# Kernel tuning notes

Hardware: AMD Instinct MI355X
Metric: run time of the kernel (lower is better)

The kernel has to match this reference:

```python
import jax, jax.numpy as jnp
import numpy as np

N_NODES = 100000
N_EDGES = 3200000
IN_DIM = 256
HID = 128
OUT = 2
BN_EPS = 1e-5


def setup_inputs() -> dict:
    key = jax.random.key(0)
    ks = jax.random.split(key, 4)
    x = jax.random.normal(ks[0], (N_NODES, IN_DIM), dtype=jnp.float32)
    edge_index = jax.random.randint(ks[1], (2, N_EDGES), 0, N_NODES, dtype=jnp.int64)
    # Glorot-ish scaled weights
    W1 = jax.random.normal(ks[2], (IN_DIM, HID), dtype=jnp.float32) * (1.0 / np.sqrt(IN_DIM))
    W2 = jax.random.normal(ks[3], (HID, OUT), dtype=jnp.float32) * (1.0 / np.sqrt(HID))
    return {
        "x": x,
        "edge_index": edge_index,
        "feature_importance": jnp.ones((IN_DIM,), jnp.float32),
        "W1": W1,
        "b1": jnp.zeros((HID,), jnp.float32),
        "W2": W2,
        "b2": jnp.zeros((OUT,), jnp.float32),
        "gamma": jnp.ones((HID,), jnp.float32),
        "beta": jnp.zeros((HID,), jnp.float32),
    }


def _gcn_conv(x, row, col, norm, W, b, n_nodes):
    # PyG GCNConv: linear transform then D^-1/2 (A+I) D^-1/2 aggregation
    h = x @ W  # [N, d_out]
    msg = h[row] * norm[:, None]  # gather + scale, [E+N, d_out]
    out = jax.ops.segment_sum(msg, col, num_segments=n_nodes)  # scatter-add
    return out + b


def _norm_and_loops(edge_index, n_nodes, dtype):
    loop = jnp.arange(n_nodes, dtype=edge_index.dtype)
    row = jnp.concatenate([edge_index[0], loop])
    col = jnp.concatenate([edge_index[1], loop])
    deg = jax.ops.segment_sum(jnp.ones_like(col, dtype=dtype), col, num_segments=n_nodes)
    dinv = jnp.where(deg > 0, jax.lax.rsqrt(deg), 0.0)
    norm = dinv[row] * dinv[col]
    return row, col, norm


def reference(x, edge_index, feature_importance, W1, b1, W2, b2, gamma, beta):
    n_nodes = x.shape[0]
    row, col, norm = _norm_and_loops(edge_index, n_nodes, x.dtype)
    # sigmoid feature-importance weighting
    xw = x * jax.nn.sigmoid(feature_importance)
    h = _gcn_conv(xw, row, col, norm, W1, b1, n_nodes)
    # BatchNorm1d with batch statistics (training-mode math; dropout omitted = eval)
    mu = jnp.mean(h, axis=0)
    var = jnp.mean((h - mu) ** 2, axis=0)
    h = (h - mu) * jax.lax.rsqrt(var + BN_EPS) * gamma + beta
    h = jax.nn.relu(h)
    out = _gcn_conv(h, row, col, norm, W2, b2, n_nodes)
    return out
```

## Files before the change

kernel.cpp:

```cpp
#include <hip/hip_runtime.h>
#include <hip/hip_bf16.h>

#define N_NODES 100000
#define N_EDGES 3200000
#define IN_DIM 256
#define HID 128
#define BN_EPS 1e-5f
#define SCAN_B 1024
#define NB1 ((N_NODES + SCAN_B - 1) / SCAN_B)


__global__ void k_deg(const int* __restrict__ col, unsigned* __restrict__ cnt) {
    int i = blockIdx.x * blockDim.x + threadIdx.x;
    if (i < N_EDGES) atomicAdd(&cnt[col[i]], 1u);
}

__global__ void k_dinv(const unsigned* __restrict__ cnt, float* __restrict__ dinv) {
    int i = blockIdx.x * blockDim.x + threadIdx.x;
    if (i < N_NODES) dinv[i] = rsqrtf((float)(cnt[i] + 1u));
}

__global__ void k_sig(const float* __restrict__ fi, float* __restrict__ sig) {
    int i = threadIdx.x;
    if (i < IN_DIM) sig[i] = 1.0f / (1.0f + expf(-fi[i]));
}


__global__ __launch_bounds__(SCAN_B) void k_scan_part(const unsigned* __restrict__ cnt,
                                                      unsigned* __restrict__ rowptr,
                                                      unsigned* __restrict__ blocksum) {
    __shared__ unsigned s[SCAN_B];
    int t = threadIdx.x;
    int i = blockIdx.x * SCAN_B + t;
    unsigned v = (i < N_NODES) ? cnt[i] : 0u;
    s[t] = v;
    __syncthreads();
#pragma unroll
    for (int off = 1; off < SCAN_B; off <<= 1) {
        unsigned u = (t >= off) ? s[t - off] : 0u;
        __syncthreads();
        s[t] += u;
        __syncthreads();
    }
    if (i < N_NODES) rowptr[i] = s[t] - v;
    if (t == SCAN_B - 1) blocksum[blockIdx.x] = s[t];
}

__global__ __launch_bounds__(128) void k_scan_mid(const unsigned* __restrict__ blocksum,
                                                  unsigned* __restrict__ blockoff) {
    __shared__ unsigned s[128];
    int t = threadIdx.x;
    unsigned v = (t < NB1) ? blocksum[t] : 0u;
    s[t] = v;
    __syncthreads();
#pragma unroll
    for (int off = 1; off < 128; off <<= 1) {
        unsigned u = (t >= off) ? s[t - off] : 0u;
        __syncthreads();
        s[t] += u;
        __syncthreads();
    }
    if (t < NB1) blockoff[t] = s[t] - v;
}

__global__ void k_scan_add(unsigned* __restrict__ rowptr, const unsigned* __restrict__ blockoff) {
    int i = blockIdx.x * blockDim.x + threadIdx.x;
    if (i < N_NODES) rowptr[i] += blockoff[i >> 10];
    if (i == 0) rowptr[N_NODES] = N_EDGES;
}


__global__ void k_bucket(const int* __restrict__ row, const int* __restrict__ col,
                         const unsigned* __restrict__ rowptr, unsigned* __restrict__ fill,
                         int* __restrict__ esrc) {
    int e = blockIdx.x * blockDim.x + threadIdx.x;
    if (e < N_EDGES) {
        int c = col[e];
        unsigned p = rowptr[c] + atomicAdd(&fill[c], 1u);
        esrc[p] = row[e];
    }
}


__global__ __launch_bounds__(256) void k_gemm1(const float* __restrict__ x,
                                               const float* __restrict__ W1,
                                               const float* __restrict__ sig,
                                               const float* __restrict__ dinv,
                                               float* __restrict__ hs) {
    __shared__ float xT[16][64];
    __shared__ float Wl[16][128];
    const int mbase = blockIdx.x * 64;
    const int t = threadIdx.x;
    const int tm = t >> 5;
    const int tn = t & 31;
    float acc[8][4] = {{0.f}};

    for (int k0 = 0; k0 < IN_DIM; k0 += 16) {
        {
            int r = t >> 2;
            int kk = (t & 3) * 4;
            int row = mbase + r;
            float4 v = make_float4(0.f, 0.f, 0.f, 0.f);
            if (row < N_NODES) v = *(const float4*)&x[row * IN_DIM + k0 + kk];
            xT[kk + 0][r] = v.x; xT[kk + 1][r] = v.y;
            xT[kk + 2][r] = v.z; xT[kk + 3][r] = v.w;
        }
        {
#pragma unroll
            for (int i = 0; i < 2; ++i) {
                int idx = t + i * 256;
                int k = idx >> 5;
                int n4 = (idx & 31) * 4;
                float4 w = *(const float4*)&W1[(k0 + k) * HID + n4];
                float s = sig[k0 + k];
                Wl[k][n4 + 0] = w.x * s; Wl[k][n4 + 1] = w.y * s;
                Wl[k][n4 + 2] = w.z * s; Wl[k][n4 + 3] = w.w * s;
            }
        }
        __syncthreads();
#pragma unroll
        for (int k = 0; k < 16; ++k) {
            float xv[8], wv[4];
            *(float4*)&xv[0] = *(const float4*)&xT[k][tm * 8];
            *(float4*)&xv[4] = *(const float4*)&xT[k][tm * 8 + 4];
            *(float4*)&wv[0] = *(const float4*)&Wl[k][tn * 4];
#pragma unroll
            for (int i = 0; i < 8; ++i)
#pragma unroll
                for (int j = 0; j < 4; ++j)
                    acc[i][j] += xv[i] * wv[j];
        }
        __syncthreads();
    }
#pragma unroll
    for (int i = 0; i < 8; ++i) {
        int row = mbase + tm * 8 + i;
        if (row < N_NODES) {
            float d = dinv[row];
            float4 v = make_float4(acc[i][0] * d, acc[i][1] * d, acc[i][2] * d, acc[i][3] * d);
            *(float4*)&hs[row * HID + tn * 4] = v;
        }
    }
}


__global__ __launch_bounds__(256) void k_agg1csr(const int* __restrict__ esrc,
                                                 const unsigned* __restrict__ rowptr,
                                                 const float* __restrict__ hs,
                                                 const float* __restrict__ dinv,
                                                 const float* __restrict__ b1,
                                                 float* __restrict__ S1,
                                                 float* __restrict__ stats) {
    const int t = threadIdx.x;
    const int lane = t & 63;
    const int gw = (blockIdx.x * blockDim.x + t) >> 6;
    const int nw = (gridDim.x * blockDim.x) >> 6;
    const int ch = lane * 2;
    const float2 bb = *(const float2*)&b1[ch];
    float s0 = 0.f, s1 = 0.f, q0 = 0.f, q1 = 0.f;

    for (int c = gw; c < N_NODES; c += nw) {
        unsigned beg = rowptr[c], end = rowptr[c + 1];
        float2 acc = *(const float2*)&hs[(size_t)c * HID + ch];
        for (unsigned base = beg; base < end; base += 64) {
            int n = (int)min(64u, end - base);
            int my = (lane < n) ? esrc[base + lane] : 0;
#pragma unroll 4
            for (int i = 0; i < n; ++i) {
                int r = __shfl(my, i);
                float2 v = *(const float2*)&hs[(size_t)r * HID + ch];
                acc.x += v.x; acc.y += v.y;
            }
        }
        float d = dinv[c];
        float v0 = d * acc.x + bb.x;
        float v1 = d * acc.y + bb.y;
        *(float2*)&S1[(size_t)c * HID + ch] = make_float2(v0, v1);
        s0 += v0; s1 += v1; q0 += v0 * v0; q1 += v1 * v1;
    }

    __shared__ float red[256];
#define RED_ATOMIC(val, idx)                                              \
    red[t] = (val); __syncthreads();                                      \
    if (t < 64) {                                                         \
        float r_ = red[t] + red[t + 64] + red[t + 128] + red[t + 192];    \
        atomicAdd(&stats[idx], r_);                                       \
    } __syncthreads();
    RED_ATOMIC(s0, ch)
    RED_ATOMIC(s1, ch + 1)
    RED_ATOMIC(q0, 128 + ch)
    RED_ATOMIC(q1, 129 + ch)
#undef RED_ATOMIC
}


__global__ void k_bnfin(const float* __restrict__ stats,
                        const float* __restrict__ gamma,
                        const float* __restrict__ beta,
                        float* __restrict__ bnp) {
    int j = threadIdx.x;
    if (j < HID) {
        float mu = stats[j] * (1.0f / N_NODES);
        float var = stats[128 + j] * (1.0f / N_NODES) - mu * mu;
        float rstd = rsqrtf(var + BN_EPS);
        float sc = rstd * gamma[j];
        bnp[j] = sc;
        bnp[128 + j] = beta[j] - mu * sc;
    }
}


__global__ __launch_bounds__(256) void k_gemm2(const float* __restrict__ S1,
                                               const float* __restrict__ bnp,
                                               const float* __restrict__ W2,
                                               const float* __restrict__ dinv,
                                               float* __restrict__ gs) {
    int wid = (blockIdx.x * blockDim.x + threadIdx.x) >> 6;
    int lane = threadIdx.x & 63;
    int nw = (gridDim.x * blockDim.x) >> 6;
    int k0 = lane * 2;
    float2 sc = *(const float2*)&bnp[k0];
    float2 sh = *(const float2*)&bnp[128 + k0];
    float4 w = *(const float4*)&W2[k0 * 2];
    for (int n = wid; n < N_NODES; n += nw) {
        float2 h = *(const float2*)&S1[(size_t)n * HID + k0];
        float v0 = fmaxf(h.x * sc.x + sh.x, 0.f);
        float v1 = fmaxf(h.y * sc.y + sh.y, 0.f);
        float a0 = v0 * w.x + v1 * w.z;
        float a1 = v0 * w.y + v1 * w.w;
#pragma unroll
        for (int off = 32; off; off >>= 1) {
            a0 += __shfl_down(a0, off);
            a1 += __shfl_down(a1, off);
        }
        if (lane == 0) {
            float d = dinv[n];
            *(float2*)&gs[n * 2] = make_float2(a0 * d, a1 * d);
        }
    }
}


__global__ void k_agg2csr(const int* __restrict__ esrc,
                          const unsigned* __restrict__ rowptr,
                          const float* __restrict__ gs,
                          const float* __restrict__ dinv,
                          const float* __restrict__ b2,
                          float* __restrict__ out) {
    int c = blockIdx.x * blockDim.x + threadIdx.x;
    if (c >= N_NODES) return;
    float2 acc = *(const float2*)&gs[c * 2];
    unsigned beg = rowptr[c], end = rowptr[c + 1];
    for (unsigned i = beg; i < end; ++i) {
        int r = esrc[i];
        float2 v = *(const float2*)&gs[r * 2];
        acc.x += v.x; acc.y += v.y;
    }
    float d = dinv[c];
    *(float2*)&out[c * 2] = make_float2(d * acc.x + b2[0], d * acc.y + b2[1]);
}


extern "C" void kernel_launch(void* const* d_in, const int* in_sizes, int n_in,
                              void* d_out, int out_size, void* d_ws, size_t ws_size,
                              hipStream_t stream) {
    const float* x     = (const float*)d_in[0];
    const int*   edge  = (const int*)d_in[1];
    const float* fi    = (const float*)d_in[2];
    const float* W1    = (const float*)d_in[3];
    const float* b1    = (const float*)d_in[4];
    const float* W2    = (const float*)d_in[5];
    const float* b2    = (const float*)d_in[6];
    const float* gamma = (const float*)d_in[7];
    const float* beta  = (const float*)d_in[8];
    float* out = (float*)d_out;

    const int* erow = edge;
    const int* ecol = edge + N_EDGES;

    char* ws = (char*)d_ws;
    size_t off = 0;
    auto alloc = [&](size_t bytes) { size_t r = off; off = (off + bytes + 255) & ~(size_t)255; return r; };
    float*    hs    = (float*)(ws + alloc(sizeof(float) * (size_t)N_NODES * HID));
    float*    S1    = (float*)(ws + alloc(sizeof(float) * (size_t)N_NODES * HID));
    int*      esrc  = (int*)(ws + alloc(sizeof(int) * (size_t)N_EDGES));
    float*    gs    = (float*)(ws + alloc(sizeof(float) * N_NODES * 2));
    unsigned* cnt   = (unsigned*)(ws + alloc(sizeof(unsigned) * N_NODES));
    unsigned* fill  = (unsigned*)(ws + alloc(sizeof(unsigned) * N_NODES));
    unsigned* rowptr= (unsigned*)(ws + alloc(sizeof(unsigned) * (N_NODES + 1)));
    unsigned* bsum  = (unsigned*)(ws + alloc(sizeof(unsigned) * NB1));
    unsigned* boff  = (unsigned*)(ws + alloc(sizeof(unsigned) * NB1));
    float*    dinv  = (float*)(ws + alloc(sizeof(float) * N_NODES));
    float*    sig   = (float*)(ws + alloc(sizeof(float) * IN_DIM));
    float*    stats = (float*)(ws + alloc(sizeof(float) * 2 * HID));
    float*    bnp   = (float*)(ws + alloc(sizeof(float) * 2 * HID));
    (void)ws_size; (void)in_sizes; (void)n_in; (void)out_size;

    hipMemsetAsync(cnt, 0, sizeof(unsigned) * N_NODES, stream);
    hipMemsetAsync(fill, 0, sizeof(unsigned) * N_NODES, stream);
    hipMemsetAsync(stats, 0, sizeof(float) * 2 * HID, stream);

    k_deg<<<(N_EDGES + 255) / 256, 256, 0, stream>>>(ecol, cnt);
    k_dinv<<<(N_NODES + 255) / 256, 256, 0, stream>>>(cnt, dinv);
    k_sig<<<1, 256, 0, stream>>>(fi, sig);

    k_scan_part<<<NB1, SCAN_B, 0, stream>>>(cnt, rowptr, bsum);
    k_scan_mid<<<1, 128, 0, stream>>>(bsum, boff);
    k_scan_add<<<(N_NODES + 255) / 256, 256, 0, stream>>>(rowptr, boff);
    k_bucket<<<(N_EDGES + 255) / 256, 256, 0, stream>>>(erow, ecol, rowptr, fill, esrc);

    k_gemm1<<<(N_NODES + 63) / 64, 256, 0, stream>>>(x, W1, sig, dinv, hs);
    k_agg1csr<<<2048, 256, 0, stream>>>(esrc, rowptr, hs, dinv, b1, S1, stats);
    k_bnfin<<<1, 128, 0, stream>>>(stats, gamma, beta, bnp);
    k_gemm2<<<2048, 256, 0, stream>>>(S1, bnp, W2, dinv, gs);
    k_agg2csr<<<(N_NODES + 255) / 256, 256, 0, stream>>>(esrc, rowptr, gs, dinv, b2, out);
}
```

Baseline: 895.6 us.

## Use bf16 MFMA for first GEMM and store hidden features as bf16

Replaces the fp32 shared-memory SIMT GEMM with bf16 MFMA 16x16x32 instructions. The sigmoid-scaled W1 is pre-transposed and converted to bf16 in a small prep kernel, and x is converted to bf16 on the fly. The hidden features hs are now written as packed bf16, which halves the bytes gathered per edge in the first aggregation, the dominant memory-bound gather over 3.2M edges. In exchange, precision drops to bf16 in both the GEMM inputs and the stored intermediate features.

Result: faster. 822.4 us (-8.2%).

```diff
diff --git a/kernel.cpp b/kernel.cpp
--- a/kernel.cpp
+++ b/kernel.cpp
@@ -9,6 +9,17 @@
 #define SCAN_B 1024
 #define NB1 ((N_NODES + SCAN_B - 1) / SCAN_B)
 
+typedef __attribute__((ext_vector_type(8))) short bf16x8;
+typedef __attribute__((ext_vector_type(4))) float f32x4;
+
+__device__ __forceinline__ ushort f2bf(float f) {
+    unsigned u = __float_as_uint(f);
+    u += 0x7FFFu + ((u >> 16) & 1u);
+    return (ushort)(u >> 16);
+}
+__device__ __forceinline__ float bflo(unsigned v) { return __uint_as_float(v << 16); }
+__device__ __forceinline__ float bfhi(unsigned v) { return __uint_as_float(v & 0xFFFF0000u); }
+
 
 __global__ void k_deg(const int* __restrict__ col, unsigned* __restrict__ cnt) {
     int i = blockIdx.x * blockDim.x + threadIdx.x;
@@ -23,6 +34,15 @@
 __global__ void k_sig(const float* __restrict__ fi, float* __restrict__ sig) {
     int i = threadIdx.x;
     if (i < IN_DIM) sig[i] = 1.0f / (1.0f + expf(-fi[i]));
+}
+
+__global__ void k_prepw(const float* __restrict__ W1, const float* __restrict__ sig,
+                        ushort* __restrict__ W1t) {
+    int idx = blockIdx.x * blockDim.x + threadIdx.x;
+    if (idx < HID * IN_DIM) {
+        int n = idx >> 8, k = idx & 255;
+        W1t[idx] = f2bf(W1[k * HID + n] * sig[k]);
+    }
 }
 
 
@@ -83,70 +103,51 @@
 
 
 __global__ __launch_bounds__(256) void k_gemm1(const float* __restrict__ x,
-                                               const float* __restrict__ W1,
-                                               const float* __restrict__ sig,
+                                               const ushort* __restrict__ W1t,
                                                const float* __restrict__ dinv,
-                                               float* __restrict__ hs) {
-    __shared__ float xT[16][64];
-    __shared__ float Wl[16][128];
-    const int mbase = blockIdx.x * 64;
+                                               unsigned* __restrict__ hsu) {
     const int t = threadIdx.x;
-    const int tm = t >> 5;
-    const int tn = t & 31;
-    float acc[8][4] = {{0.f}};
-
-    for (int k0 = 0; k0 < IN_DIM; k0 += 16) {
-        {
-            int r = t >> 2;
-            int kk = (t & 3) * 4;
-            int row = mbase + r;
-            float4 v = make_float4(0.f, 0.f, 0.f, 0.f);
-            if (row < N_NODES) v = *(const float4*)&x[row * IN_DIM + k0 + kk];
-            xT[kk + 0][r] = v.x; xT[kk + 1][r] = v.y;
-            xT[kk + 2][r] = v.z; xT[kk + 3][r] = v.w;
+    const int w = (blockIdx.x << 2) + (t >> 6);
+    const int m0 = w << 4;
+    if (m0 >= N_NODES) return;
+    const int lane = t & 63;
+    const int mrow = lane & 15;
+    const int quad = lane >> 4;
+
+    const float* xrow = x + (size_t)(m0 + mrow) * IN_DIM + quad * 8;
+    const ushort* wrow = W1t + mrow * IN_DIM + quad * 8;
+
+    f32x4 acc[8] = {};
+#pragma unroll
+    for (int ks = 0; ks < 8; ++ks) {
+        float4 xa = *(const float4*)(xrow + ks * 32);
+        float4 xb = *(const float4*)(xrow + ks * 32 + 4);
+        bf16x8 bfrag;
+        bfrag[0] = (short)f2bf(xa.x); bfrag[1] = (short)f2bf(xa.y);
+        bfrag[2] = (short)f2bf(xa.z); bfrag[3] = (short)f2bf(xa.w);
+        bfrag[4] = (short)f2bf(xb.x); bfrag[5] = (short)f2bf(xb.y);
+        bfrag[6] = (short)f2bf(xb.z); bfrag[7] = (short)f2bf(xb.w);
+        const ushort* wk = wrow + ks * 32;
+#pragma unroll
+        for (int nb = 0; nb < 8; ++nb) {
+            bf16x8 afrag = *(const bf16x8*)(wk + nb * 16 * IN_DIM);
+            acc[nb] = __builtin_amdgcn_mfma_f32_16x16x32_bf16(afrag, bfrag, acc[nb], 0, 0, 0);
         }
-        {
-#pragma unroll
-            for (int i = 0; i < 2; ++i) {
-                int idx = t + i * 256;
-                int k = idx >> 5;
-                int n4 = (idx & 31) * 4;
-                float4 w = *(const float4*)&W1[(k0 + k) * HID + n4];
-                float s = sig[k0 + k];
-                Wl[k][n4 + 0] = w.x * s; Wl[k][n4 + 1] = w.y * s;
-                Wl[k][n4 + 2] = w.z * s; Wl[k][n4 + 3] = w.w * s;
-            }
-        }
-        __syncthreads();
-#pragma unroll
-        for (int k = 0; k < 16; ++k) {
-            float xv[8], wv[4];
-            *(float4*)&xv[0] = *(const float4*)&xT[k][tm * 8];
-            *(float4*)&xv[4] = *(const float4*)&xT[k][tm * 8 + 4];
-            *(float4*)&wv[0] = *(const float4*)&Wl[k][tn * 4];
-#pragma unroll
-            for (int i = 0; i < 8; ++i)
-#pragma unroll
-                for (int j = 0; j < 4; ++j)
-                    acc[i][j] += xv[i] * wv[j];
-        }
-        __syncthreads();
-    }
-#pragma unroll
-    for (int i = 0; i < 8; ++i) {
-        int row = mbase + tm * 8 + i;
-        if (row < N_NODES) {
-            float d = dinv[row];
-            float4 v = make_float4(acc[i][0] * d, acc[i][1] * d, acc[i][2] * d, acc[i][3] * d);
-            *(float4*)&hs[row * HID + tn * 4] = v;
-        }
+    }
+    const float d = dinv[m0 + mrow];
+    unsigned* orow = hsu + (size_t)(m0 + mrow) * 64;
+#pragma unroll
+    for (int nb = 0; nb < 8; ++nb) {
+        unsigned p0 = (unsigned)f2bf(acc[nb][0] * d) | ((unsigned)f2bf(acc[nb][1] * d) << 16);
+        unsigned p1 = (unsigned)f2bf(acc[nb][2] * d) | ((unsigned)f2bf(acc[nb][3] * d) << 16);
+        *(uint2*)(orow + nb * 8 + quad * 2) = make_uint2(p0, p1);
     }
 }
 
 
 __global__ __launch_bounds__(256) void k_agg1csr(const int* __restrict__ esrc,
                                                  const unsigned* __restrict__ rowptr,
-                                                 const float* __restrict__ hs,
+                                                 const unsigned* __restrict__ hsu,
                                                  const float* __restrict__ dinv,
                                                  const float* __restrict__ b1,
                                                  float* __restrict__ S1,
@@ -161,20 +162,21 @@
 
     for (int c = gw; c < N_NODES; c += nw) {
         unsigned beg = rowptr[c], end = rowptr[c + 1];
-        float2 acc = *(const float2*)&hs[(size_t)c * HID + ch];
+        unsigned self = hsu[(size_t)c * 64 + lane];
+        float a0 = bflo(self), a1 = bfhi(self);
         for (unsigned base = beg; base < end; base += 64) {
             int n = (int)min(64u, end - base);
             int my = (lane < n) ? esrc[base + lane] : 0;
 #pragma unroll 4
             for (int i = 0; i < n; ++i) {
                 int r = __shfl(my, i);
-                float2 v = *(const float2*)&hs[(size_t)r * HID + ch];
-                acc.x += v.x; acc.y += v.y;
+                unsigned v = hsu[(size_t)r * 64 + lane];
+                a0 += bflo(v); a1 += bfhi(v);
             }
         }
         float d = dinv[c];
-        float v0 = d * acc.x + bb.x;
-        float v1 = d * acc.y + bb.y;
+        float v0 = d * a0 + bb.x;
+        float v1 = d * a1 + bb.y;
         *(float2*)&S1[(size_t)c * HID + ch] = make_float2(v0, v1);
         s0 += v0; s1 += v1; q0 += v0 * v0; q1 += v1 * v1;
     }
@@ -281,7 +283,7 @@
     char* ws = (char*)d_ws;
     size_t off = 0;
     auto alloc = [&](size_t bytes) { size_t r = off; off = (off + bytes + 255) & ~(size_t)255; return r; };
-    float*    hs    = (float*)(ws + alloc(sizeof(float) * (size_t)N_NODES * HID));
+    unsigned* hsu   = (unsigned*)(ws + alloc(sizeof(unsigned) * (size_t)N_NODES * 64));
     float*    S1    = (float*)(ws + alloc(sizeof(float) * (size_t)N_NODES * HID));
     int*      esrc  = (int*)(ws + alloc(sizeof(int) * (size_t)N_EDGES));
     float*    gs    = (float*)(ws + alloc(sizeof(float) * N_NODES * 2));
@@ -292,6 +294,7 @@
     unsigned* boff  = (unsigned*)(ws + alloc(sizeof(unsigned) * NB1));
     float*    dinv  = (float*)(ws + alloc(sizeof(float) * N_NODES));
     float*    sig   = (float*)(ws + alloc(sizeof(float) * IN_DIM));
+    ushort*   W1t   = (ushort*)(ws + alloc(sizeof(ushort) * HID * IN_DIM));
     float*    stats = (float*)(ws + alloc(sizeof(float) * 2 * HID));
     float*    bnp   = (float*)(ws + alloc(sizeof(float) * 2 * HID));
     (void)ws_size; (void)in_sizes; (void)n_in; (void)out_size;
@@ -303,14 +306,15 @@
     k_deg<<<(N_EDGES + 255) / 256, 256, 0, stream>>>(ecol, cnt);
     k_dinv<<<(N_NODES + 255) / 256, 256, 0, stream>>>(cnt, dinv);
     k_sig<<<1, 256, 0, stream>>>(fi, sig);
+    k_prepw<<<(HID * IN_DIM + 255) / 256, 256, 0, stream>>>(W1, sig, W1t);
 
     k_scan_part<<<NB1, SCAN_B, 0, stream>>>(cnt, rowptr, bsum);
     k_scan_mid<<<1, 128, 0, stream>>>(bsum, boff);
     k_scan_add<<<(N_NODES + 255) / 256, 256, 0, stream>>>(rowptr, boff);
     k_bucket<<<(N_EDGES + 255) / 256, 256, 0, stream>>>(erow, ecol, rowptr, fill, esrc);
 
-    k_gemm1<<<(N_NODES + 63) / 64, 256, 0, stream>>>(x, W1, sig, dinv, hs);
-    k_agg1csr<<<2048, 256, 0, stream>>>(esrc, rowptr, hs, dinv, b1, S1, stats);
+    k_gemm1<<<(N_NODES / 16 + 3) / 4, 256, 0, stream>>>(x, W1t, dinv, hsu);
+    k_agg1csr<<<2048, 256, 0, stream>>>(esrc, rowptr, hsu, dinv, b1, S1, stats);
     k_bnfin<<<1, 128, 0, stream>>>(stats, gamma, beta, bnp);
     k_gemm2<<<2048, 256, 0, stream>>>(S1, bnp, W2, dinv, gs);
     k_agg2csr<<<(N_NODES + 255) / 256, 256, 0, stream>>>(esrc, rowptr, gs, dinv, b2, out);
```
